# Optimization experiments

Hardware: AMD Instinct MI355X
Metric: run time of the kernel (lower is better)

## Reference

```python
import jax, jax.numpy as jnp
import numpy as np

G, N, E, F = 1000, 256, 1024, 128
D1, D2, K1, K2 = 128, 64, 32, 8
MACRO_D, LABELS, ME = 128, 10, 16000


def gcn_conv(x, src, dst, W, b):
    """PyG GCNConv: add self-loops, symmetric deg normalization, XW aggregate."""
    n = x.shape[0]
    loop = jnp.arange(n)
    s = jnp.concatenate([src, loop])
    d = jnp.concatenate([dst, loop])
    deg = jax.ops.segment_sum(jnp.ones_like(s, dtype=x.dtype), d, num_segments=n)
    dinv = jax.lax.rsqrt(jnp.maximum(deg, 1e-12))  # deg >= 1 due to self-loops
    norm = dinv[s] * dinv[d]                        # [E+n]
    xw = x @ W                                      # [n, out]
    msg = xw[s] * norm[:, None]
    return jax.ops.segment_sum(msg, d, num_segments=n) + b


def setup_inputs() -> dict:
    key = jax.random.key(0)
    ks = jax.random.split(key, 12)
    g = lambda k, shp, fan: (jax.random.normal(k, shp, jnp.float32) / np.sqrt(fan)).astype(jnp.float32)
    return {
        "graph_features": jax.random.normal(ks[0], (G, N, F), jnp.float32),
        "graph_edges": jax.random.randint(ks[1], (G, 2, E), 0, N),
        "macro_edges": jax.random.randint(ks[2], (2, ME), 0, G),
        "W1": g(ks[3], (F, D1), F), "b1": jnp.zeros((D1,), jnp.float32),
        "W2": g(ks[4], (D1, D2), D1), "b2": jnp.zeros((D2,), jnp.float32),
        "Wf1": g(ks[5], (D2, K1), D2), "bf1": jnp.zeros((K1,), jnp.float32),
        "Wf2": g(ks[6], (K1, K2), K1), "bf2": jnp.zeros((K2,), jnp.float32),
        "Wm1": g(ks[7], (D2 * K2, MACRO_D), D2 * K2), "bm1": jnp.zeros((MACRO_D,), jnp.float32),
        "Wm2": g(ks[8], (MACRO_D, LABELS), MACRO_D), "bm2": jnp.zeros((LABELS,), jnp.float32),
    }


def reference(graph_features, graph_edges, macro_edges,
              W1, b1, W2, b2, Wf1, bf1, Wf2, bf2, Wm1, bm1, Wm2, bm2):
    def sage(x, edges):
        src, dst = edges[0], edges[1]
        h1 = jax.nn.relu(gcn_conv(x, src, dst, W1, b1))      # [N, D1]
        h2 = gcn_conv(h1, src, dst, W2, b2)                  # [N, D2]
        a = jnp.tanh(h2 @ Wf1 + bf1)                         # [N, K1]
        att = jax.nn.softmax(a @ Wf2 + bf2, axis=0)          # softmax over nodes, [N, K2]
        emb = (att.T @ h2).reshape(-1)                       # [K2*D2]
        P = att.T @ att - jnp.eye(K2, dtype=x.dtype)         # [K2, K2]
        pen = jnp.sum(jnp.sqrt(jnp.sum(P * P, axis=1)))      # sum of row L2 norms
        return emb, pen

    embs, pens = jax.vmap(sage)(graph_features, graph_edges)  # [G, K2*D2], [G]
    penalty = jnp.mean(pens)

    msrc, mdst = macro_edges[0], macro_edges[1]
    h = jax.nn.relu(gcn_conv(embs, msrc, mdst, Wm1, bm1))     # [G, MACRO_D]
    logits = gcn_conv(h, msrc, mdst, Wm2, bm2)                # [G, LABELS]
    predictions = jax.nn.log_softmax(logits, axis=1)
    return predictions, penalty
```

## Files before the change

### kernel.cpp

```cpp
#include <hip/hip_runtime.h>
#include <math.h>

typedef __attribute__((ext_vector_type(8))) short short8;
typedef __attribute__((ext_vector_type(4))) float f32x4;

#define G_ 1000
#define N_ 256
#define E_ 1024
#define F_ 128
#define D1_ 128
#define D2_ 64
#define K1_ 32
#define K2_ 8
#define MD_ 128
#define LB_ 10
#define ME_ 16000

#define OFS_PEN   0
#define OFS_CNT   4
#define OFS_DINVM 1004
#define OFS_EMB   2004
#define OFS_XW1M  514004
#define OFS_HM    642004
#define OFS_XW2M  770004
#define OFS_LOGM  780004
#define OFS_WFRAG 790016

static __device__ __forceinline__ unsigned short f2bf(float f) {
  unsigned u = __builtin_bit_cast(unsigned, f);
  u += 0x7fff + ((u >> 16) & 1);
  return (unsigned short)(u >> 16);
}
static __device__ __forceinline__ float bf2f(unsigned short h) {
  return __builtin_bit_cast(float, (unsigned)h << 16);
}

__global__ __launch_bounds__(256)
void init_kernel(float* ws) {
  int i = blockIdx.x * 256 + threadIdx.x;
  if (i == 0) ws[OFS_PEN] = 0.f;
  if (i < 1000) ((int*)(ws + OFS_CNT))[i] = 0;
}

__global__ __launch_bounds__(256)
void prep_kernel(const float* __restrict__ W1, const float* __restrict__ W2,
                 unsigned short* __restrict__ w1f, unsigned short* __restrict__ w2f) {
  int t = blockIdx.x * 256 + threadIdx.x;
  for (int idx = t; idx < 8 * 4 * 64 * 8; idx += gridDim.x * 256) {
    int j = idx & 7, l = (idx >> 3) & 63, ks = (idx >> 9) & 3, nt = idx >> 11;
    w1f[idx] = f2bf(W1[(ks * 32 + (l >> 4) * 8 + j) * D1_ + nt * 16 + (l & 15)]);
  }
  for (int idx = t; idx < 4 * 4 * 64 * 8; idx += gridDim.x * 256) {
    int j = idx & 7, l = (idx >> 3) & 63, ks = (idx >> 9) & 3, nt = idx >> 11;
    w2f[idx] = f2bf(W2[(ks * 32 + (l >> 4) * 8 + j) * D2_ + nt * 16 + (l & 15)]);
  }
}

__global__ __launch_bounds__(512, 4)
void graph_kernel(const float* __restrict__ X, const int* __restrict__ GE,
                  const unsigned short* __restrict__ W1F, const unsigned short* __restrict__ W2F,
                  const float* __restrict__ b1, const float* __restrict__ b2,
                  const float* __restrict__ Wf1, const float* __restrict__ bf1,
                  const float* __restrict__ Wf2, const float* __restrict__ bf2,
                  float* __restrict__ ws)
{
  extern __shared__ unsigned char smemraw[];
  unsigned short* chunkA = (unsigned short*)smemraw;
  unsigned short* h2s    = chunkA + 256 * 40;
  float* enorm  = (float*)(h2s + 256 * 72);
  int*   rowst  = (int*)(enorm + 1024);
  int*   fill   = rowst + 256;
  float* dinv_s = (float*)(fill + 256);
  float* red    = dinv_s + 256;
  unsigned short* esrc = (unsigned short*)(red + 96);
  float* att_s = (float*)chunkA;
  float* wf1s  = (float*)chunkA + 2048;
  float* wf2s  = (float*)chunkA + 4096;

  const int g = blockIdx.x, tid = threadIdx.x;
  const int w = tid >> 6, lane = tid & 63;
  const int l15 = lane & 15, l4 = lane >> 4;
  const float* xg = X + (size_t)g * (N_ * F_);
  const int*   esG = GE + (size_t)g * (2 * E_);

  if (tid < 256) fill[tid] = 0;
  __syncthreads();
  int s0 = esG[tid * 2], d0 = esG[E_ + tid * 2];
  int s1 = esG[tid * 2 + 1], d1 = esG[E_ + tid * 2 + 1];
  atomicAdd(&fill[d0], 1);
  atomicAdd(&fill[d1], 1);
  __syncthreads();
  int myrow = 0;
  if (tid < 256) {
    int deg = fill[tid];
    dinv_s[tid] = rsqrtf((float)deg + 1.f);
    int v = deg;
#pragma unroll
    for (int off = 1; off < 64; off <<= 1) {
      int u = __shfl_up(v, off);
      if (lane >= off) v += u;
    }
    if (lane == 63) ((int*)red)[w] = v;
    myrow = v - deg;
  }
  __syncthreads();
  if (tid < 256) {
    int pre = 0;
#pragma unroll
    for (int q = 0; q < 4; ++q) if (q < w) pre += ((int*)red)[q];
    rowst[tid] = myrow + pre;
    fill[tid] = 0;
  }
  __syncthreads();
  {
    int pos = rowst[d0] + atomicAdd(&fill[d0], 1);
    esrc[pos] = (unsigned short)s0;
    enorm[pos] = dinv_s[s0] * dinv_s[d0];
    pos = rowst[d1] + atomicAdd(&fill[d1], 1);
    esrc[pos] = (unsigned short)s1;
    enorm[pos] = dinv_s[s1] * dinv_s[d1];
  }
  __syncthreads();

  const int nd = tid >> 1, jhalf = tid & 1;
  const int rb = rowst[nd], rc = fill[nd];
  const float dii = dinv_s[nd] * dinv_s[nd];

  short8 xA[2][4];
#pragma unroll
  for (int mt = 0; mt < 2; ++mt) {
    const float* xr = xg + (w * 32 + mt * 16 + l15) * F_ + l4 * 8;
#pragma unroll
    for (int ks = 0; ks < 4; ++ks) {
      float4 u = *(const float4*)(xr + ks * 32);
      float4 v2 = *(const float4*)(xr + ks * 32 + 4);
      short8 t;
      t[0] = (short)f2bf(u.x);  t[1] = (short)f2bf(u.y);
      t[2] = (short)f2bf(u.z);  t[3] = (short)f2bf(u.w);
      t[4] = (short)f2bf(v2.x); t[5] = (short)f2bf(v2.y);
      t[6] = (short)f2bf(v2.z); t[7] = (short)f2bf(v2.w);
      xA[mt][ks] = t;
    }
  }

  f32x4 acc2[2][4];
#pragma unroll
  for (int mt = 0; mt < 2; ++mt)
#pragma unroll
    for (int nt = 0; nt < 4; ++nt) acc2[mt][nt] = (f32x4){0.f, 0.f, 0.f, 0.f};

  for (int c = 0; c < 4; ++c) {
    __syncthreads();
    f32x4 acc1[2][2];
#pragma unroll
    for (int mt = 0; mt < 2; ++mt) { acc1[mt][0] = (f32x4){0.f,0.f,0.f,0.f}; acc1[mt][1] = (f32x4){0.f,0.f,0.f,0.f}; }
#pragma unroll
    for (int ks = 0; ks < 4; ++ks) {
      short8 bA = *(const short8*)(W1F + (((2 * c + 0) * 4 + ks) * 64 + lane) * 8);
      short8 bB = *(const short8*)(W1F + (((2 * c + 1) * 4 + ks) * 64 + lane) * 8);
#pragma unroll
      for (int mt = 0; mt < 2; ++mt) {
        acc1[mt][0] = __builtin_amdgcn_mfma_f32_16x16x32_bf16(xA[mt][ks], bA, acc1[mt][0], 0, 0, 0);
        acc1[mt][1] = __builtin_amdgcn_mfma_f32_16x16x32_bf16(xA[mt][ks], bB, acc1[mt][1], 0, 0, 0);
      }
    }
#pragma unroll
    for (int mt = 0; mt < 2; ++mt)
#pragma unroll
      for (int ntl = 0; ntl < 2; ++ntl)
#pragma unroll
        for (int r = 0; r < 4; ++r)
          chunkA[(w * 32 + mt * 16 + l4 * 4 + r) * 40 + ntl * 16 + l15] = f2bf(acc1[mt][ntl][r]);
    __syncthreads();
    float gacc[16];
    {
      const unsigned short* rp = chunkA + nd * 40 + jhalf * 16;
      short8 v0 = *(const short8*)(rp);
      short8 v1 = *(const short8*)(rp + 8);
#pragma unroll
      for (int j = 0; j < 8; ++j) {
        gacc[j]     = dii * bf2f((unsigned short)v0[j]);
        gacc[8 + j] = dii * bf2f((unsigned short)v1[j]);
      }
    }
    for (int e = 0; e < rc; ++e) {
      int s = esrc[rb + e]; float nm = enorm[rb + e];
      const unsigned short* sp = chunkA + s * 40 + jhalf * 16;
      short8 v0 = *(const short8*)(sp);
      short8 v1 = *(const short8*)(sp + 8);
#pragma unroll
      for (int j = 0; j < 8; ++j) {
        gacc[j]     = fmaf(nm, bf2f((unsigned short)v0[j]), gacc[j]);
        gacc[8 + j] = fmaf(nm, bf2f((unsigned short)v1[j]), gacc[8 + j]);
      }
    }
    const float* bp = b1 + c * 32 + jhalf * 16;
    __syncthreads();
    {
      short8 o0, o1;
#pragma unroll
      for (int j = 0; j < 8; ++j) {
        o0[j] = (short)f2bf(fmaxf(gacc[j] + bp[j], 0.f));
        o1[j] = (short)f2bf(fmaxf(gacc[8 + j] + bp[8 + j], 0.f));
      }
      *(short8*)(chunkA + nd * 40 + jhalf * 16) = o0;
      *(short8*)(chunkA + nd * 40 + jhalf * 16 + 8) = o1;
    }
    __syncthreads();
    {
      short8 hA0 = *(const short8*)(chunkA + (w * 32 + 0 * 16 + l15) * 40 + l4 * 8);
      short8 hA1 = *(const short8*)(chunkA + (w * 32 + 1 * 16 + l15) * 40 + l4 * 8);
#pragma unroll
      for (int nt = 0; nt < 4; ++nt) {
        short8 bf = *(const short8*)(W2F + ((nt * 4 + c) * 64 + lane) * 8);
        acc2[0][nt] = __builtin_amdgcn_mfma_f32_16x16x32_bf16(hA0, bf, acc2[0][nt], 0, 0, 0);
        acc2[1][nt] = __builtin_amdgcn_mfma_f32_16x16x32_bf16(hA1, bf, acc2[1][nt], 0, 0, 0);
      }
    }
  }

#pragma unroll
  for (int mt = 0; mt < 2; ++mt)
#pragma unroll
    for (int nt = 0; nt < 4; ++nt)
#pragma unroll
      for (int r = 0; r < 4; ++r)
        h2s[(w * 32 + mt * 16 + l4 * 4 + r) * 72 + nt * 16 + l15] = f2bf(acc2[mt][nt][r]);
  __syncthreads();
  float g2[32];
  {
    const unsigned short* rp = h2s + nd * 72 + jhalf * 32;
#pragma unroll
    for (int q = 0; q < 4; ++q) {
      short8 v = *(const short8*)(rp + q * 8);
#pragma unroll
      for (int j = 0; j < 8; ++j) g2[q * 8 + j] = dii * bf2f((unsigned short)v[j]);
    }
  }
  for (int e = 0; e < rc; ++e) {
    int s = esrc[rb + e]; float nm = enorm[rb + e];
    const unsigned short* sp = h2s + s * 72 + jhalf * 32;
#pragma unroll
    for (int q = 0; q < 4; ++q) {
      short8 v = *(const short8*)(sp + q * 8);
#pragma unroll
      for (int j = 0; j < 8; ++j) g2[q * 8 + j] = fmaf(nm, bf2f((unsigned short)v[j]), g2[q * 8 + j]);
    }
  }
  const float* b2p = b2 + jhalf * 32;
  __syncthreads();
  {
#pragma unroll
    for (int q = 0; q < 4; ++q) {
      short8 o;
#pragma unroll
      for (int j = 0; j < 8; ++j) o[j] = (short)f2bf(g2[q * 8 + j] + b2p[q * 8 + j]);
      *(short8*)(h2s + nd * 72 + jhalf * 32 + q * 8) = o;
    }
  }
  for (int i = tid; i < 2048; i += 512) wf1s[i] = Wf1[i];
  if (tid < 256) wf2s[tid] = Wf2[tid];
  __syncthreads();

  float l_r[8], ex8[8];
  if (tid < 256) {
    float a_r[32];
#pragma unroll
    for (int j = 0; j < 32; ++j) a_r[j] = bf1[j];
    const unsigned short* hrow = h2s + tid * 72;
    for (int d = 0; d < 64; d += 8) {
      short8 hv8 = *(const short8*)(hrow + d);
#pragma unroll
      for (int dj = 0; dj < 8; ++dj) {
        float hv = bf2f((unsigned short)hv8[dj]);
        const float* wr = wf1s + (d + dj) * K1_;
#pragma unroll
        for (int j4 = 0; j4 < 8; ++j4) {
          float4 wv = *(const float4*)(wr + j4 * 4);
          a_r[j4 * 4 + 0] = fmaf(hv, wv.x, a_r[j4 * 4 + 0]);
          a_r[j4 * 4 + 1] = fmaf(hv, wv.y, a_r[j4 * 4 + 1]);
          a_r[j4 * 4 + 2] = fmaf(hv, wv.z, a_r[j4 * 4 + 2]);
          a_r[j4 * 4 + 3] = fmaf(hv, wv.w, a_r[j4 * 4 + 3]);
        }
      }
    }
#pragma unroll
    for (int j = 0; j < 32; ++j) a_r[j] = tanhf(a_r[j]);
#pragma unroll
    for (int jj = 0; jj < 8; ++jj) l_r[jj] = bf2[jj];
#pragma unroll
    for (int j = 0; j < 32; ++j) {
      float av = a_r[j];
      const float* wr = wf2s + j * K2_;
#pragma unroll
      for (int jj = 0; jj < 8; ++jj) l_r[jj] = fmaf(av, wr[jj], l_r[jj]);
    }
    float mx[8];
#pragma unroll
    for (int jj = 0; jj < 8; ++jj) mx[jj] = l_r[jj];
#pragma unroll
    for (int off = 1; off < 64; off <<= 1)
#pragma unroll
      for (int jj = 0; jj < 8; ++jj) mx[jj] = fmaxf(mx[jj], __shfl_xor(mx[jj], off));
    if (lane == 0)
#pragma unroll
      for (int jj = 0; jj < 8; ++jj) red[w * 8 + jj] = mx[jj];
  }
  __syncthreads();
  if (tid < 256) {
#pragma unroll
    for (int jj = 0; jj < 8; ++jj) {
      float m = fmaxf(fmaxf(red[jj], red[8 + jj]), fmaxf(red[16 + jj], red[24 + jj]));
      ex8[jj] = expf(l_r[jj] - m);
    }
    float sm[8];
#pragma unroll
    for (int jj = 0; jj < 8; ++jj) sm[jj] = ex8[jj];
#pragma unroll
    for (int off = 1; off < 64; off <<= 1)
#pragma unroll
      for (int jj = 0; jj < 8; ++jj) sm[jj] += __shfl_xor(sm[jj], off);
    if (lane == 0)
#pragma unroll
      for (int jj = 0; jj < 8; ++jj) red[32 + w * 8 + jj] = sm[jj];
  }
  __syncthreads();
  if (tid < 256) {
#pragma unroll
    for (int jj = 0; jj < 8; ++jj) {
      float tot = red[32 + jj] + red[40 + jj] + red[48 + jj] + red[56 + jj];
      att_s[tid * 8 + jj] = ex8[jj] / tot;
    }
  }
  __syncthreads();

  {
    int jj = tid >> 6, d = tid & 63;
    float acc = 0.f;
    for (int i = 0; i < 256; ++i)
      acc = fmaf(att_s[i * 8 + jj], bf2f(h2s[i * 72 + d]), acc);
    ws[OFS_EMB + (size_t)g * 512 + jj * 64 + d] = acc;
  }

  if (tid < 64) {
    int j = tid >> 3, k = tid & 7;
    float acc = 0.f;
    for (int i = 0; i < 256; ++i) acc += att_s[i * 8 + j] * att_s[i * 8 + k];
    if (j == k) acc -= 1.f;
    red[tid] = acc * acc;
  }
  __syncthreads();
  if (tid < 8) {
    float s2 = 0.f;
#pragma unroll
    for (int k = 0; k < 8; ++k) s2 += red[tid * 8 + k];
    red[64 + tid] = sqrtf(s2);
  }
  __syncthreads();
  if (tid == 0) {
    float p = 0.f;
#pragma unroll
    for (int k = 0; k < 8; ++k) p += red[64 + k];
    atomicAdd(&ws[OFS_PEN], p);
  }
}

__global__ __launch_bounds__(256)
void mcount_kernel(const int* __restrict__ me, float* ws) {
  int i = blockIdx.x * 256 + threadIdx.x;
  if (i < ME_) atomicAdd(&((int*)(ws + OFS_CNT))[me[ME_ + i]], 1);
}

__global__ __launch_bounds__(256)
void mdinv_kernel(float* ws) {
  int i = blockIdx.x * 256 + threadIdx.x;
  if (i < 1000) ws[OFS_DINVM + i] = rsqrtf((float)((int*)(ws + OFS_CNT))[i] + 1.0f);
}

__global__ __launch_bounds__(128)
void m1_kernel(const float* __restrict__ Wm1, const float* __restrict__ bm1, float* ws) {
  __shared__ float er[512];
  int g = blockIdx.x, t = threadIdx.x;
  const float* eg = ws + OFS_EMB + (size_t)g * 512;
  *reinterpret_cast<float4*>(&er[t * 4]) = *reinterpret_cast<const float4*>(&eg[t * 4]);
  __syncthreads();
  float acc = 0.f;
#pragma unroll 4
  for (int k = 0; k < 512; ++k) acc += er[k] * Wm1[k * MD_ + t];
  float dm = ws[OFS_DINVM + g];
  ws[OFS_XW1M + g * MD_ + t] = acc;
  ws[OFS_HM   + g * MD_ + t] = acc * dm * dm + bm1[t];
}

__global__ __launch_bounds__(128)
void m2_kernel(const int* __restrict__ me, float* ws) {
  int e = blockIdx.x, t = threadIdx.x;
  int s = me[e], d = me[ME_ + e];
  float nm = ws[OFS_DINVM + s] * ws[OFS_DINVM + d];
  atomicAdd(&ws[OFS_HM + d * MD_ + t], ws[OFS_XW1M + s * MD_ + t] * nm);
}

__global__ __launch_bounds__(128)
void m3_kernel(const float* __restrict__ Wm2, const float* __restrict__ bm2, float* ws) {
  __shared__ float hr[128];
  int g = blockIdx.x, t = threadIdx.x;
  hr[t] = fmaxf(ws[OFS_HM + g * MD_ + t], 0.f);
  __syncthreads();
  if (t < LB_) {
    float acc = 0.f;
#pragma unroll 4
    for (int k = 0; k < 128; ++k) acc += hr[k] * Wm2[k * LB_ + t];
    float dm = ws[OFS_DINVM + g];
    ws[OFS_XW2M + g * LB_ + t] = acc;
    ws[OFS_LOGM + g * LB_ + t] = acc * dm * dm + bm2[t];
  }
}

__global__ __launch_bounds__(256)
void m4_kernel(const int* __restrict__ me, float* ws) {
  int idx = blockIdx.x * 256 + threadIdx.x;
  if (idx < ME_ * LB_) {
    int e = idx / LB_, j = idx - e * LB_;
    int s = me[e], d = me[ME_ + e];
    float nm = ws[OFS_DINVM + s] * ws[OFS_DINVM + d];
    atomicAdd(&ws[OFS_LOGM + d * LB_ + j], ws[OFS_XW2M + s * LB_ + j] * nm);
  }
}

__global__ __launch_bounds__(64)
void m5_kernel(const float* __restrict__ ws, float* __restrict__ out) {
  int g = blockIdx.x;
  if (threadIdx.x == 0) {
    float v[10];
    float mx = -1e30f;
#pragma unroll
    for (int j = 0; j < LB_; ++j) { v[j] = ws[OFS_LOGM + g * LB_ + j]; mx = fmaxf(mx, v[j]); }
    float se = 0.f;
#pragma unroll
    for (int j = 0; j < LB_; ++j) se += expf(v[j] - mx);
    float lse = mx + logf(se);
#pragma unroll
    for (int j = 0; j < LB_; ++j) out[g * LB_ + j] = v[j] - lse;
  }
  if (g == 0 && threadIdx.x == 1) out[10000] = ws[OFS_PEN] * 0.001f;
}

extern "C" void kernel_launch(void* const* d_in, const int* in_sizes, int n_in,
                              void* d_out, int out_size, void* d_ws, size_t ws_size,
                              hipStream_t stream)
{
  const float* X   = (const float*)d_in[0];
  const int*   GE  = (const int*)d_in[1];
  const int*   MEe = (const int*)d_in[2];
  const float* W1  = (const float*)d_in[3];
  const float* b1  = (const float*)d_in[4];
  const float* W2  = (const float*)d_in[5];
  const float* b2  = (const float*)d_in[6];
  const float* Wf1 = (const float*)d_in[7];
  const float* bf1 = (const float*)d_in[8];
  const float* Wf2 = (const float*)d_in[9];
  const float* bf2 = (const float*)d_in[10];
  const float* Wm1 = (const float*)d_in[11];
  const float* bm1 = (const float*)d_in[12];
  const float* Wm2 = (const float*)d_in[13];
  const float* bm2 = (const float*)d_in[14];
  float* ws  = (float*)d_ws;
  float* out = (float*)d_out;

  unsigned short* w1f = (unsigned short*)(ws + OFS_WFRAG);
  unsigned short* w2f = w1f + 16384;

  prep_kernel<<<32, 256, 0, stream>>>(W1, W2, w1f, w2f);
  init_kernel<<<5, 256, 0, stream>>>(ws);

  size_t lds = 66944;
  graph_kernel<<<G_, 512, lds, stream>>>(X, GE, w1f, w2f, b1, b2, Wf1, bf1, Wf2, bf2, ws);

  mcount_kernel<<<(ME_ + 255) / 256, 256, 0, stream>>>(MEe, ws);
  mdinv_kernel<<<4, 256, 0, stream>>>(ws);
  m1_kernel<<<G_, 128, 0, stream>>>(Wm1, bm1, ws);
  m2_kernel<<<ME_, 128, 0, stream>>>(MEe, ws);
  m3_kernel<<<G_, 128, 0, stream>>>(Wm2, bm2, ws);
  m4_kernel<<<(ME_ * LB_ + 255) / 256, 256, 0, stream>>>(MEe, ws);
  m5_kernel<<<G_, 64, 0, stream>>>(ws, out);
}
```

Baseline: 413.3 us.

## Use MFMA for attention projections and CSR gather for macro GCN

The per-node Wf1 projection, the attention-weighted embedding and the att^T att penalty Gram matrix now run on bf16 MFMA. Split hi/lo bf16 pairs keep them close to fp32 accuracy, and a transposed h2 copy is stored in LDS for the embedding product. The macro-graph GCN replaces per-edge atomic scatter kernels with a single-block CSR build and gather-based aggregation, fusing the layers into fewer launches. LDS use rises to about 80 KB per block, which may lower occupancy of the graph kernel.

```diff
diff --git a/kernel.cpp b/kernel.cpp
--- a/kernel.cpp
+++ b/kernel.cpp
@@ -16,15 +16,15 @@
 #define LB_ 10
 #define ME_ 16000
 
-#define OFS_PEN   0
-#define OFS_CNT   4
-#define OFS_DINVM 1004
-#define OFS_EMB   2004
-#define OFS_XW1M  514004
-#define OFS_HM    642004
-#define OFS_XW2M  770004
-#define OFS_LOGM  780004
-#define OFS_WFRAG 790016
+#define OFS_PEN    0
+#define OFS_EMB    16
+#define OFS_XW1M   512016
+#define OFS_XW2M   640016
+#define OFS_DINVM  650016
+#define OFS_WNORM  651016
+#define OFS_ROWSTM 667016
+#define OFS_WSRC   668032
+#define OFS_WFRAG  676032
 
 static __device__ __forceinline__ unsigned short f2bf(float f) {
   unsigned u = __builtin_bit_cast(unsigned, f);
@@ -36,46 +36,58 @@
 }
 
 __global__ __launch_bounds__(256)
-void init_kernel(float* ws) {
-  int i = blockIdx.x * 256 + threadIdx.x;
-  if (i == 0) ws[OFS_PEN] = 0.f;
-  if (i < 1000) ((int*)(ws + OFS_CNT))[i] = 0;
-}
-
-__global__ __launch_bounds__(256)
 void prep_kernel(const float* __restrict__ W1, const float* __restrict__ W2,
-                 unsigned short* __restrict__ w1f, unsigned short* __restrict__ w2f) {
+                 const float* __restrict__ Wf1,
+                 unsigned short* __restrict__ frag, float* __restrict__ ws) {
   int t = blockIdx.x * 256 + threadIdx.x;
-  for (int idx = t; idx < 8 * 4 * 64 * 8; idx += gridDim.x * 256) {
+  if (t == 0) ws[OFS_PEN] = 0.f;
+  unsigned short* w1f  = frag;
+  unsigned short* w2f  = frag + 16384;
+  unsigned short* wf1h = frag + 24576;
+  unsigned short* wf1l = frag + 26624;
+  for (int idx = t; idx < 16384; idx += gridDim.x * 256) {
     int j = idx & 7, l = (idx >> 3) & 63, ks = (idx >> 9) & 3, nt = idx >> 11;
     w1f[idx] = f2bf(W1[(ks * 32 + (l >> 4) * 8 + j) * D1_ + nt * 16 + (l & 15)]);
   }
-  for (int idx = t; idx < 4 * 4 * 64 * 8; idx += gridDim.x * 256) {
+  for (int idx = t; idx < 8192; idx += gridDim.x * 256) {
     int j = idx & 7, l = (idx >> 3) & 63, ks = (idx >> 9) & 3, nt = idx >> 11;
     w2f[idx] = f2bf(W2[(ks * 32 + (l >> 4) * 8 + j) * D2_ + nt * 16 + (l & 15)]);
   }
+  for (int idx = t; idx < 2048; idx += gridDim.x * 256) {
+    int j = idx & 7, l = (idx >> 3) & 63, ks = (idx >> 9) & 1, nt = idx >> 10;
+    float v = Wf1[(ks * 32 + (l >> 4) * 8 + j) * K1_ + nt * 16 + (l & 15)];
+    unsigned short hi = f2bf(v);
+    wf1h[idx] = hi;
+    wf1l[idx] = f2bf(v - bf2f(hi));
+  }
 }
 
 __global__ __launch_bounds__(512, 4)
 void graph_kernel(const float* __restrict__ X, const int* __restrict__ GE,
-                  const unsigned short* __restrict__ W1F, const unsigned short* __restrict__ W2F,
+                  const unsigned short* __restrict__ FR,
                   const float* __restrict__ b1, const float* __restrict__ b2,
-                  const float* __restrict__ Wf1, const float* __restrict__ bf1,
-                  const float* __restrict__ Wf2, const float* __restrict__ bf2,
+                  const float* __restrict__ bf1, const float* __restrict__ bf2,
+                  const float* __restrict__ Wf2,
                   float* __restrict__ ws)
 {
+  const unsigned short* W1F  = FR;
+  const unsigned short* W2F  = FR + 16384;
+  const unsigned short* Wf1H = FR + 24576;
+  const unsigned short* Wf1L = FR + 26624;
+
   extern __shared__ unsigned char smemraw[];
   unsigned short* chunkA = (unsigned short*)smemraw;
-  unsigned short* h2s    = chunkA + 256 * 40;
-  float* enorm  = (float*)(h2s + 256 * 72);
-  int*   rowst  = (int*)(enorm + 1024);
-  int*   fill   = rowst + 256;
-  float* dinv_s = (float*)(fill + 256);
-  float* red    = dinv_s + 256;
-  unsigned short* esrc = (unsigned short*)(red + 96);
-  float* att_s = (float*)chunkA;
-  float* wf1s  = (float*)chunkA + 2048;
-  float* wf2s  = (float*)chunkA + 4096;
+  unsigned short* h2T    = (unsigned short*)smemraw;
+  unsigned short* h2s  = (unsigned short*)(smemraw + 33792);
+  float*          a_stf = (float*)(smemraw + 33792);
+  float*          enorm  = (float*)(smemraw + 70656);
+  unsigned short* att_hi = (unsigned short*)(smemraw + 70656);
+  unsigned short* att_lo = (unsigned short*)(smemraw + 74880);
+  unsigned short* esrc   = (unsigned short*)(smemraw + 74752);
+  int*            rowst  = (int*)(smemraw + 76800);
+  int*            fill   = (int*)(smemraw + 77824);
+  float*          dinv_s = (float*)(smemraw + 78848);
+  float*          red    = (float*)(smemraw + 79872);
 
   const int g = blockIdx.x, tid = threadIdx.x;
   const int w = tid >> 6, lane = tid & 63;
@@ -257,47 +269,58 @@
       for (int j = 0; j < 8; ++j) o[j] = (short)f2bf(g2[q * 8 + j] + b2p[q * 8 + j]);
       *(short8*)(h2s + nd * 72 + jhalf * 32 + q * 8) = o;
     }
-  }
-  for (int i = tid; i < 2048; i += 512) wf1s[i] = Wf1[i];
-  if (tid < 256) wf2s[tid] = Wf2[tid];
-  __syncthreads();
-
-  float l_r[8], ex8[8];
+#pragma unroll
+    for (int i = 0; i < 32; ++i)
+      h2T[(jhalf * 32 + i) * 264 + nd] = f2bf(g2[i] + b2p[i]);
+  }
+  __syncthreads();
+
+  short8 hA[2][2];
+#pragma unroll
+  for (int mt = 0; mt < 2; ++mt)
+#pragma unroll
+    for (int ks = 0; ks < 2; ++ks)
+      hA[mt][ks] = *(const short8*)(h2s + (w * 32 + mt * 16 + l15) * 72 + ks * 32 + l4 * 8);
+  f32x4 aacc[2][2];
+#pragma unroll
+  for (int mt = 0; mt < 2; ++mt) { aacc[mt][0] = (f32x4){0.f,0.f,0.f,0.f}; aacc[mt][1] = (f32x4){0.f,0.f,0.f,0.f}; }
+#pragma unroll
+  for (int ks = 0; ks < 2; ++ks)
+#pragma unroll
+    for (int nt = 0; nt < 2; ++nt) {
+      short8 bh = *(const short8*)(Wf1H + ((nt * 2 + ks) * 64 + lane) * 8);
+      short8 bl = *(const short8*)(Wf1L + ((nt * 2 + ks) * 64 + lane) * 8);
+#pragma unroll
+      for (int mt = 0; mt < 2; ++mt) {
+        aacc[mt][nt] = __builtin_amdgcn_mfma_f32_16x16x32_bf16(hA[mt][ks], bh, aacc[mt][nt], 0, 0, 0);
+        aacc[mt][nt] = __builtin_amdgcn_mfma_f32_16x16x32_bf16(hA[mt][ks], bl, aacc[mt][nt], 0, 0, 0);
+      }
+    }
+  __syncthreads();
+#pragma unroll
+  for (int mt = 0; mt < 2; ++mt)
+#pragma unroll
+    for (int nt = 0; nt < 2; ++nt)
+#pragma unroll
+      for (int r = 0; r < 4; ++r)
+        a_stf[(w * 32 + mt * 16 + l4 * 4 + r) * 34 + nt * 16 + l15] =
+            tanhf(aacc[mt][nt][r] + bf1[nt * 16 + l15]);
+  __syncthreads();
+
+  float lv[8], ex[8];
   if (tid < 256) {
-    float a_r[32];
-#pragma unroll
-    for (int j = 0; j < 32; ++j) a_r[j] = bf1[j];
-    const unsigned short* hrow = h2s + tid * 72;
-    for (int d = 0; d < 64; d += 8) {
-      short8 hv8 = *(const short8*)(hrow + d);
-#pragma unroll
-      for (int dj = 0; dj < 8; ++dj) {
-        float hv = bf2f((unsigned short)hv8[dj]);
-        const float* wr = wf1s + (d + dj) * K1_;
-#pragma unroll
-        for (int j4 = 0; j4 < 8; ++j4) {
-          float4 wv = *(const float4*)(wr + j4 * 4);
-          a_r[j4 * 4 + 0] = fmaf(hv, wv.x, a_r[j4 * 4 + 0]);
-          a_r[j4 * 4 + 1] = fmaf(hv, wv.y, a_r[j4 * 4 + 1]);
-          a_r[j4 * 4 + 2] = fmaf(hv, wv.z, a_r[j4 * 4 + 2]);
-          a_r[j4 * 4 + 3] = fmaf(hv, wv.w, a_r[j4 * 4 + 3]);
-        }
-      }
-    }
-#pragma unroll
-    for (int j = 0; j < 32; ++j) a_r[j] = tanhf(a_r[j]);
-#pragma unroll
-    for (int jj = 0; jj < 8; ++jj) l_r[jj] = bf2[jj];
-#pragma unroll
+#pragma unroll
+    for (int jj = 0; jj < 8; ++jj) lv[jj] = bf2[jj];
+    const float* ar = a_stf + tid * 34;
     for (int j = 0; j < 32; ++j) {
-      float av = a_r[j];
-      const float* wr = wf2s + j * K2_;
-#pragma unroll
-      for (int jj = 0; jj < 8; ++jj) l_r[jj] = fmaf(av, wr[jj], l_r[jj]);
+      float av = ar[j];
+      const float* wr = Wf2 + j * K2_;
+#pragma unroll
+      for (int jj = 0; jj < 8; ++jj) lv[jj] = fmaf(av, wr[jj], lv[jj]);
     }
     float mx[8];
 #pragma unroll
-    for (int jj = 0; jj < 8; ++jj) mx[jj] = l_r[jj];
+    for (int jj = 0; jj < 8; ++jj) mx[jj] = lv[jj];
 #pragma unroll
     for (int off = 1; off < 64; off <<= 1)
 #pragma unroll
@@ -311,11 +334,11 @@
 #pragma unroll
     for (int jj = 0; jj < 8; ++jj) {
       float m = fmaxf(fmaxf(red[jj], red[8 + jj]), fmaxf(red[16 + jj], red[24 + jj]));
-      ex8[jj] = expf(l_r[jj] - m);
+      ex[jj] = expf(lv[jj] - m);
     }
     float sm[8];
 #pragma unroll
-    for (int jj = 0; jj < 8; ++jj) sm[jj] = ex8[jj];
+    for (int jj = 0; jj < 8; ++jj) sm[jj] = ex[jj];
 #pragma unroll
     for (int off = 1; off < 64; off <<= 1)
 #pragma unroll
@@ -329,120 +352,167 @@
 #pragma unroll
     for (int jj = 0; jj < 8; ++jj) {
       float tot = red[32 + jj] + red[40 + jj] + red[48 + jj] + red[56 + jj];
-      att_s[tid * 8 + jj] = ex8[jj] / tot;
-    }
-  }
-  __syncthreads();
-
-  {
-    int jj = tid >> 6, d = tid & 63;
-    float acc = 0.f;
-    for (int i = 0; i < 256; ++i)
-      acc = fmaf(att_s[i * 8 + jj], bf2f(h2s[i * 72 + d]), acc);
-    ws[OFS_EMB + (size_t)g * 512 + jj * 64 + d] = acc;
-  }
-
-  if (tid < 64) {
-    int j = tid >> 3, k = tid & 7;
-    float acc = 0.f;
-    for (int i = 0; i < 256; ++i) acc += att_s[i * 8 + j] * att_s[i * 8 + k];
-    if (j == k) acc -= 1.f;
-    red[tid] = acc * acc;
+      float av = ex[jj] / tot;
+      unsigned short hi = f2bf(av);
+      att_hi[jj * 264 + tid] = hi;
+      att_lo[jj * 264 + tid] = f2bf(av - bf2f(hi));
+    }
+  }
+  __syncthreads();
+
+  const int rl = l15 & 7;
+  if (w < 4) {
+    f32x4 d = (f32x4){0.f, 0.f, 0.f, 0.f};
+#pragma unroll
+    for (int ks = 0; ks < 8; ++ks) {
+      short8 ah = *(const short8*)(att_hi + rl * 264 + ks * 32 + l4 * 8);
+      short8 al = *(const short8*)(att_lo + rl * 264 + ks * 32 + l4 * 8);
+      short8 bv = *(const short8*)(h2T + (w * 16 + l15) * 264 + ks * 32 + l4 * 8);
+      d = __builtin_amdgcn_mfma_f32_16x16x32_bf16(ah, bv, d, 0, 0, 0);
+      d = __builtin_amdgcn_mfma_f32_16x16x32_bf16(al, bv, d, 0, 0, 0);
+    }
+    if (l4 < 2) {
+      float* eg = ws + OFS_EMB + (size_t)g * 512;
+#pragma unroll
+      for (int r = 0; r < 4; ++r)
+        eg[(l4 * 4 + r) * 64 + w * 16 + l15] = d[r];
+    }
+  } else if (w == 4) {
+    f32x4 p = (f32x4){0.f, 0.f, 0.f, 0.f};
+#pragma unroll
+    for (int ks = 0; ks < 8; ++ks) {
+      short8 ah = *(const short8*)(att_hi + rl * 264 + ks * 32 + l4 * 8);
+      short8 al = *(const short8*)(att_lo + rl * 264 + ks * 32 + l4 * 8);
+      p = __builtin_amdgcn_mfma_f32_16x16x32_bf16(ah, ah, p, 0, 0, 0);
+      p = __builtin_amdgcn_mfma_f32_16x16x32_bf16(ah, al, p, 0, 0, 0);
+      p = __builtin_amdgcn_mfma_f32_16x16x32_bf16(al, ah, p, 0, 0, 0);
+    }
+    if (l4 < 2 && l15 < 8) {
+#pragma unroll
+      for (int r = 0; r < 4; ++r) {
+        float v = p[r];
+        if (l4 * 4 + r == l15) v -= 1.f;
+        red[64 + (l4 * 4 + r) * 8 + l15] = v * v;
+      }
+    }
   }
   __syncthreads();
   if (tid < 8) {
     float s2 = 0.f;
 #pragma unroll
-    for (int k = 0; k < 8; ++k) s2 += red[tid * 8 + k];
-    red[64 + tid] = sqrtf(s2);
+    for (int k = 0; k < 8; ++k) s2 += red[64 + tid * 8 + k];
+    red[128 + tid] = sqrtf(s2);
   }
   __syncthreads();
   if (tid == 0) {
     float p = 0.f;
 #pragma unroll
-    for (int k = 0; k < 8; ++k) p += red[64 + k];
+    for (int k = 0; k < 8; ++k) p += red[128 + k];
     atomicAdd(&ws[OFS_PEN], p);
   }
 }
 
-__global__ __launch_bounds__(256)
-void mcount_kernel(const int* __restrict__ me, float* ws) {
-  int i = blockIdx.x * 256 + threadIdx.x;
-  if (i < ME_) atomicAdd(&((int*)(ws + OFS_CNT))[me[ME_ + i]], 1);
-}
-
-__global__ __launch_bounds__(256)
-void mdinv_kernel(float* ws) {
-  int i = blockIdx.x * 256 + threadIdx.x;
-  if (i < 1000) ws[OFS_DINVM + i] = rsqrtf((float)((int*)(ws + OFS_CNT))[i] + 1.0f);
+__global__ __launch_bounds__(1024)
+void macro_csr(const int* __restrict__ me, float* __restrict__ ws) {
+  __shared__ int cnt[1000];
+  __shared__ float dinvL[1000];
+  __shared__ int wtot[16];
+  int t = threadIdx.x, lane = t & 63, wv = t >> 6;
+  for (int i = t; i < 1000; i += 1024) cnt[i] = 0;
+  __syncthreads();
+  for (int e = t; e < ME_; e += 1024) atomicAdd(&cnt[me[ME_ + e]], 1);
+  __syncthreads();
+  int v = (t < 1000) ? cnt[t] : 0;
+  float di = rsqrtf((float)v + 1.f);
+  if (t < 1000) { dinvL[t] = di; ws[OFS_DINVM + t] = di; }
+  int sc = v;
+#pragma unroll
+  for (int off = 1; off < 64; off <<= 1) {
+    int u = __shfl_up(sc, off);
+    if (lane >= off) sc += u;
+  }
+  if (lane == 63) wtot[wv] = sc;
+  __syncthreads();
+  int pre = 0;
+#pragma unroll
+  for (int q = 0; q < 16; ++q) if (q < wv) pre += wtot[q];
+  int rs = pre + sc - v;
+  int* rowstM = (int*)(ws + OFS_ROWSTM);
+  if (t < 1000) rowstM[t] = rs;
+  if (t == 0) rowstM[1000] = ME_;
+  __syncthreads();
+  if (t < 1000) cnt[t] = rs;
+  __syncthreads();
+  unsigned short* wsrc = (unsigned short*)(ws + OFS_WSRC);
+  for (int e = t; e < ME_; e += 1024) {
+    int s = me[e], d = me[ME_ + e];
+    int pos = atomicAdd(&cnt[d], 1);
+    wsrc[pos] = (unsigned short)s;
+    ws[OFS_WNORM + pos] = dinvL[s] * dinvL[d];
+  }
 }
 
 __global__ __launch_bounds__(128)
-void m1_kernel(const float* __restrict__ Wm1, const float* __restrict__ bm1, float* ws) {
+void macro1(const float* __restrict__ Wm1, float* __restrict__ ws) {
   __shared__ float er[512];
   int g = blockIdx.x, t = threadIdx.x;
-  const float* eg = ws + OFS_EMB + (size_t)g * 512;
-  *reinterpret_cast<float4*>(&er[t * 4]) = *reinterpret_cast<const float4*>(&eg[t * 4]);
+  *(float4*)&er[t * 4] = *(const float4*)&ws[OFS_EMB + (size_t)g * 512 + t * 4];
   __syncthreads();
   float acc = 0.f;
 #pragma unroll 4
-  for (int k = 0; k < 512; ++k) acc += er[k] * Wm1[k * MD_ + t];
-  float dm = ws[OFS_DINVM + g];
+  for (int k = 0; k < 512; ++k) acc = fmaf(er[k], Wm1[k * MD_ + t], acc);
   ws[OFS_XW1M + g * MD_ + t] = acc;
-  ws[OFS_HM   + g * MD_ + t] = acc * dm * dm + bm1[t];
 }
 
 __global__ __launch_bounds__(128)
-void m2_kernel(const int* __restrict__ me, float* ws) {
-  int e = blockIdx.x, t = threadIdx.x;
-  int s = me[e], d = me[ME_ + e];
-  float nm = ws[OFS_DINVM + s] * ws[OFS_DINVM + d];
-  atomicAdd(&ws[OFS_HM + d * MD_ + t], ws[OFS_XW1M + s * MD_ + t] * nm);
-}
-
-__global__ __launch_bounds__(128)
-void m3_kernel(const float* __restrict__ Wm2, const float* __restrict__ bm2, float* ws) {
-  __shared__ float hr[128];
+void macro2(const float* __restrict__ bm1, const float* __restrict__ Wm2, float* __restrict__ ws) {
+  __shared__ float wred[2][10];
   int g = blockIdx.x, t = threadIdx.x;
-  hr[t] = fmaxf(ws[OFS_HM + g * MD_ + t], 0.f);
-  __syncthreads();
-  if (t < LB_) {
-    float acc = 0.f;
-#pragma unroll 4
-    for (int k = 0; k < 128; ++k) acc += hr[k] * Wm2[k * LB_ + t];
-    float dm = ws[OFS_DINVM + g];
-    ws[OFS_XW2M + g * LB_ + t] = acc;
-    ws[OFS_LOGM + g * LB_ + t] = acc * dm * dm + bm2[t];
-  }
-}
-
-__global__ __launch_bounds__(256)
-void m4_kernel(const int* __restrict__ me, float* ws) {
-  int idx = blockIdx.x * 256 + threadIdx.x;
-  if (idx < ME_ * LB_) {
-    int e = idx / LB_, j = idx - e * LB_;
-    int s = me[e], d = me[ME_ + e];
-    float nm = ws[OFS_DINVM + s] * ws[OFS_DINVM + d];
-    atomicAdd(&ws[OFS_LOGM + d * LB_ + j], ws[OFS_XW2M + s * LB_ + j] * nm);
-  }
+  const int* rowstM = (const int*)(ws + OFS_ROWSTM);
+  const unsigned short* wsrc = (const unsigned short*)(ws + OFS_WSRC);
+  int e0 = rowstM[g], e1 = rowstM[g + 1];
+  float di = ws[OFS_DINVM + g];
+  float acc = di * di * ws[OFS_XW1M + g * MD_ + t];
+  for (int e = e0; e < e1; ++e)
+    acc = fmaf(ws[OFS_WNORM + e], ws[OFS_XW1M + (int)wsrc[e] * MD_ + t], acc);
+  float hv = fmaxf(acc + bm1[t], 0.f);
+  float part[10];
+#pragma unroll
+  for (int j = 0; j < 10; ++j) part[j] = hv * Wm2[t * LB_ + j];
+#pragma unroll
+  for (int off = 1; off < 64; off <<= 1)
+#pragma unroll
+    for (int j = 0; j < 10; ++j) part[j] += __shfl_xor(part[j], off);
+  if ((t & 63) == 0)
+#pragma unroll
+    for (int j = 0; j < 10; ++j) wred[t >> 6][j] = part[j];
+  __syncthreads();
+  if (t < 10) ws[OFS_XW2M + g * LB_ + t] = wred[0][t] + wred[1][t];
 }
 
 __global__ __launch_bounds__(64)
-void m5_kernel(const float* __restrict__ ws, float* __restrict__ out) {
-  int g = blockIdx.x;
-  if (threadIdx.x == 0) {
-    float v[10];
-    float mx = -1e30f;
-#pragma unroll
-    for (int j = 0; j < LB_; ++j) { v[j] = ws[OFS_LOGM + g * LB_ + j]; mx = fmaxf(mx, v[j]); }
-    float se = 0.f;
-#pragma unroll
-    for (int j = 0; j < LB_; ++j) se += expf(v[j] - mx);
-    float lse = mx + logf(se);
-#pragma unroll
-    for (int j = 0; j < LB_; ++j) out[g * LB_ + j] = v[j] - lse;
-  }
-  if (g == 0 && threadIdx.x == 1) out[10000] = ws[OFS_PEN] * 0.001f;
+void macro3(const float* __restrict__ bm2, const float* __restrict__ ws, float* __restrict__ out) {
+  int g = blockIdx.x, t = threadIdx.x;
+  const int* rowstM = (const int*)(ws + OFS_ROWSTM);
+  const unsigned short* wsrc = (const unsigned short*)(ws + OFS_WSRC);
+  int e0 = rowstM[g], e1 = rowstM[g + 1];
+  float di = ws[OFS_DINVM + g];
+  float lg = -1e30f;
+  if (t < 10) {
+    float acc = di * di * ws[OFS_XW2M + g * LB_ + t];
+    for (int e = e0; e < e1; ++e)
+      acc = fmaf(ws[OFS_WNORM + e], ws[OFS_XW2M + (int)wsrc[e] * LB_ + t], acc);
+    lg = acc + bm2[t];
+  }
+  float m = lg;
+#pragma unroll
+  for (int off = 1; off < 16; off <<= 1) m = fmaxf(m, __shfl_xor(m, off));
+  float e_ = (t < 10) ? expf(lg - m) : 0.f;
+  float s = e_;
+#pragma unroll
+  for (int off = 1; off < 16; off <<= 1) s += __shfl_xor(s, off);
+  if (t < 10) out[g * LB_ + t] = lg - m - logf(s);
+  if (g == 0 && t == 63) out[10000] = ws[OFS_PEN] * 0.001f;
 }
 
 extern "C" void kernel_launch(void* const* d_in, const int* in_sizes, int n_in,
@@ -467,20 +537,15 @@
   float* ws  = (float*)d_ws;
   float* out = (float*)d_out;
 
-  unsigned short* w1f = (unsigned short*)(ws + OFS_WFRAG);
-  unsigned short* w2f = w1f + 16384;
-
-  prep_kernel<<<32, 256, 0, stream>>>(W1, W2, w1f, w2f);
-  init_kernel<<<5, 256, 0, stream>>>(ws);
-
-  size_t lds = 66944;
-  graph_kernel<<<G_, 512, lds, stream>>>(X, GE, w1f, w2f, b1, b2, Wf1, bf1, Wf2, bf2, ws);
-
-  mcount_kernel<<<(ME_ + 255) / 256, 256, 0, stream>>>(MEe, ws);
-  mdinv_kernel<<<4, 256, 0, stream>>>(ws);
-  m1_kernel<<<G_, 128, 0, stream>>>(Wm1, bm1, ws);
-  m2_kernel<<<ME_, 128, 0, stream>>>(MEe, ws);
-  m3_kernel<<<G_, 128, 0, stream>>>(Wm2, bm2, ws);
-  m4_kernel<<<(ME_ * LB_ + 255) / 256, 256, 0, stream>>>(MEe, ws);
-  m5_kernel<<<G_, 64, 0, stream>>>(ws, out);
-}
+  unsigned short* frag = (unsigned short*)(ws + OFS_WFRAG);
+
+  prep_kernel<<<32, 256, 0, stream>>>(W1, W2, Wf1, frag, ws);
+  macro_csr<<<1, 1024, 0, stream>>>(MEe, ws);
+
+  size_t lds = 80896;
+  graph_kernel<<<G_, 512, lds, stream>>>(X, GE, frag, b1, b2, bf1, bf2, Wf2, ws);
+
+  macro1<<<G_, 128, 0, stream>>>(Wm1, ws);
+  macro2<<<G_, 128, 0, stream>>>(bm1, Wm2, ws);
+  macro3<<<G_, 64, 0, stream>>>(bm2, ws, out);
+}
```

Result: no change. 417.6 us (+1.1%).
